# Performance work log

Hardware: AMD Instinct MI355X
Metric: run time of the kernel (lower is better)

The kernel has to match this reference:

```python
import jax, jax.numpy as jnp
import numpy as np

# ---- static config (from init_kwargs) ----
SAMPLE_RATE = 2048.0
MAX_SHIFT = int(0.025 * SAMPLE_RATE)          # 51 samples
NUM_BINS = 16
FFTLENGTH = 1.0                               # chisq_kernel_length (s)
DF = 1.0 / FFTLENGTH
NUM_FREQS = int(FFTLENGTH * SAMPLE_RATE // 2 + 1)   # 1025 == rfft bins of 2048 samples
HIGHPASS = 32.0
CHISQ_PENALTY = 1.0
_freqs = np.arange(NUM_FREQS) / FFTLENGTH
MASK = _freqs >= HIGHPASS                     # static numpy bool mask

BATCH, CHANNELS, DIM = 256, 2, 2048


def setup_inputs() -> dict:
    key = jax.random.key(0)
    k1, k2 = jax.random.split(key)
    x_hat = jax.random.normal(k1, (BATCH, CHANNELS, DIM), dtype=jnp.float32)
    x = jax.random.normal(k2, (BATCH, CHANNELS, DIM), dtype=jnp.float32)
    return {"x_hat": x_hat, "x": x}


def _center(x):
    xmin = x.min(-1, keepdims=True)
    xmax = x.max(-1, keepdims=True)
    return 2 * (x - xmin) / (xmax - xmin) - 1


def _shifted_pearson(x, y, max_shift):
    # x, y: [B, C, T]; returns corr: [W, B, C] with W = 2*max_shift + 1
    b, c, t = x.shape
    num_windows = 2 * max_shift + 1
    xp = jnp.pad(x, ((0, 0), (0, 0), (max_shift, max_shift)))
    # window w, position i -> xp[..., i + w]  (same layout as torch unfold)
    idx = jnp.arange(num_windows)[:, None] + jnp.arange(t)[None, :]   # [W, T]
    xw = xp[:, :, idx]                                                # [B, C, W, T]
    xw = jnp.transpose(xw, (2, 0, 1, 3))                              # [W, B, C, T]
    xw = xw - xw.mean(-1, keepdims=True)
    yc = y - y.mean(-1, keepdims=True)
    corr = (xw * yc).sum(-1)
    norm = (xw ** 2).sum(-1) * (yc ** 2).sum(-1)
    return corr / jnp.sqrt(norm)


def _snr_integral(a, b):
    # |4 * a * conj(b) * df| cumulatively summed over frequency
    integrand = a * jnp.conj(b)
    return jnp.abs(4 * integrand * DF).cumsum(-1)


def _chisq(htilde, stilde):
    htilde = htilde[:, :, MASK]
    stilde = stilde[:, :, MASK]
    # partition frequencies by the template's own optimal-SNR integral
    si = _snr_integral(htilde, htilde)                    # [B, C, F]
    total = si[:, :, -1:]
    bins = (jnp.arange(NUM_BINS + 1, dtype=si.dtype) / NUM_BINS) * total  # [B, C, NB+1]
    search = jax.vmap(jax.vmap(lambda a, v: jnp.searchsorted(a, v, side="right")))
    edges = search(si, bins)
    edges = jnp.clip(edges, 0, si.shape[-1] - 1)
    qtilde = htilde / jnp.sqrt(total).astype(htilde.dtype)
    # SNR per bin of the normalized template against the strain
    si2 = _snr_integral(qtilde, stilde)                   # [B, C, F]
    total2 = si2[:, :, -1:]
    right = jnp.take_along_axis(si2, edges[:, :, 1:], axis=-1)
    left = jnp.take_along_axis(si2, edges[:, :, :-1], axis=-1)
    snr_per_bin = right - left                            # [B, C, NB]
    summand = (snr_per_bin - total2 / NUM_BINS) ** 2
    chisq = NUM_BINS * summand.sum(-1) / (NUM_BINS - 1)
    return total2[:, :, 0], chisq


def reference(x_hat, x):
    x_hat = _center(x_hat)
    corr = _shifted_pearson(x_hat, x, MAX_SHIFT)          # [W, B, C]
    corr = corr.max(0)                                    # [B, C]
    loss = (1 - corr) / (1 + corr)
    htilde = jnp.fft.rfft(x_hat, axis=-1) / SAMPLE_RATE   # [B, C, 1025] complex
    stilde = jnp.fft.rfft(x, axis=-1) / SAMPLE_RATE
    _, chisq = _chisq(htilde, stilde)
    chisq = chisq * CHISQ_PENALTY
    loss = loss * (1 + chisq ** 3) ** (1.0 / 6.0)
    return loss
```

## Files before the change

### kernel.cpp

```cpp
#include <hip/hip_runtime.h>
#include <math.h>

#define ROWS 512
#define DIM 2048
#define MS 51
#define NWIN 103
#define KMIN 32
#define NMASK 993
#define PHYS(i) ((i) + ((i) >> 5))

__global__ __launch_bounds__(512) void fused_mfl_kernel(
    const float* __restrict__ xhat, const float* __restrict__ x,
    float* __restrict__ out)
{
    const int r = blockIdx.x;
    const int t = threadIdx.x;
    const int lane = t & 63;
    const int wave = t >> 6;
    const float* xh = xhat + (size_t)r * DIM;
    const float* xr = x + (size_t)r * DIM;

    __shared__ float smem[16384];
    float* red6  = smem;
    float* yh    = smem;
    float* yc    = smem + 2224;
    float* headS = smem + 4352;
    float* headQ = smem + 4404;
    float* tailS = smem + 4456;
    float* tailQ = smem + 4508;
    float* V     = smem + 9216;
    float* corrv = smem + 16220;
    float2* A  = (float2*)smem;
    float2* Bb = (float2*)(smem + 4096);
    float2* TW = (float2*)(smem + 8192);
    float* siA  = smem;
    float* siBr = smem + 1024;

    __shared__ float sc[8];
    __shared__ int   edges[17];
    __shared__ float summ[16];
    __shared__ float wsA[8], wsB[8];

    float4 a4 = ((const float4*)xh)[t];
    float4 b4 = ((const float4*)xr)[t];
    float av[4] = {a4.x, a4.y, a4.z, a4.w};
    float bv[4] = {b4.x, b4.y, b4.z, b4.w};

    {
        float swv, cwv;
        sincosf((float)t * (-3.14159265358979323846f / 1024.0f), &swv, &cwv);
        TW[t] = make_float2(cwv, swv);
    }

    {
        float mn4 = fminf(fminf(av[0], av[1]), fminf(av[2], av[3]));
        float mx4 = fmaxf(fmaxf(av[0], av[1]), fmaxf(av[2], av[3]));
        float sa = (av[0] + av[1]) + (av[2] + av[3]);
        float qa = (av[0]*av[0] + av[1]*av[1]) + (av[2]*av[2] + av[3]*av[3]);
        float sx = (bv[0] + bv[1]) + (bv[2] + bv[3]);
        float qx = (bv[0]*bv[0] + bv[1]*bv[1]) + (bv[2]*bv[2] + bv[3]*bv[3]);
        red6[t]        = mn4;
        red6[512 + t]  = mx4;
        red6[1024 + t] = sa;
        red6[1536 + t] = qa;
        red6[2048 + t] = sx;
        red6[2560 + t] = qx;
    }
    __syncthreads();
    if (wave == 0) {
        float4 u, v;
        u = ((const float4*)(red6       ))[2*lane]; v = ((const float4*)(red6       ))[2*lane+1];
        float pmn = fminf(fminf(fminf(u.x,u.y),fminf(u.z,u.w)),
                          fminf(fminf(v.x,v.y),fminf(v.z,v.w)));
        u = ((const float4*)(red6 +  512))[2*lane]; v = ((const float4*)(red6 +  512))[2*lane+1];
        float pmx = fmaxf(fmaxf(fmaxf(u.x,u.y),fmaxf(u.z,u.w)),
                          fmaxf(fmaxf(v.x,v.y),fmaxf(v.z,v.w)));
        u = ((const float4*)(red6 + 1024))[2*lane]; v = ((const float4*)(red6 + 1024))[2*lane+1];
        float psa = ((u.x+u.y)+(u.z+u.w)) + ((v.x+v.y)+(v.z+v.w));
        u = ((const float4*)(red6 + 1536))[2*lane]; v = ((const float4*)(red6 + 1536))[2*lane+1];
        float pqa = ((u.x+u.y)+(u.z+u.w)) + ((v.x+v.y)+(v.z+v.w));
        u = ((const float4*)(red6 + 2048))[2*lane]; v = ((const float4*)(red6 + 2048))[2*lane+1];
        float psx = ((u.x+u.y)+(u.z+u.w)) + ((v.x+v.y)+(v.z+v.w));
        u = ((const float4*)(red6 + 2560))[2*lane]; v = ((const float4*)(red6 + 2560))[2*lane+1];
        float pqx = ((u.x+u.y)+(u.z+u.w)) + ((v.x+v.y)+(v.z+v.w));
#pragma unroll
        for (int d = 32; d; d >>= 1) {
            pmn = fminf(pmn, __shfl_down(pmn, d));
            pmx = fmaxf(pmx, __shfl_down(pmx, d));
            psa += __shfl_down(psa, d);
            pqa += __shfl_down(pqa, d);
            psx += __shfl_down(psx, d);
            pqx += __shfl_down(pqx, d);
        }
        if (lane == 0) {
            float mn = pmn, mx = pmx;
            float scl = 2.0f / (mx - mn);
            float mean = psx * (1.0f / DIM);
            float Sm = psa - (float)DIM * mn;
            float S1 = scl * Sm - (float)DIM;
            float S2 = scl * scl * (pqa - 2.f * mn * psa + (float)DIM * mn * mn)
                     - 2.f * scl * Sm + (float)DIM;
            float Syy = pqx - (float)DIM * mean * mean;
            sc[0] = mn; sc[1] = scl; sc[2] = mean;
            sc[3] = S1; sc[4] = S2; sc[5] = Syy;
        }
    }
    __syncthreads();
    const float mnv = sc[0], scl = sc[1], mean = sc[2];
    const float S1 = sc[3], S2 = sc[4], Syy = sc[5];

    float yhv[4];
#pragma unroll
    for (int j = 0; j < 4; ++j) {
        float y = (av[j] - mnv) * scl - 1.0f;
        float z = bv[j] - mean;
        yhv[j] = y;
        int i = 4 * t + j;
        yh[PHYS(i + MS)] = y;
        yc[PHYS(i)] = z;
    }
    if (t < MS) { yh[PHYS(t)] = 0.f; yh[PHYS(t + MS + DIM)] = 0.f; }
    __syncthreads();

    if (wave < 2) {
        float v = 0.f;
        if (lane >= 1 && lane <= MS)
            v = (wave == 0) ? yh[PHYS(MS + lane - 1)] : yh[PHYS(MS + DIM - lane)];
        float s = v, q = v * v;
#pragma unroll
        for (int d = 1; d < 64; d <<= 1) {
            float ys = __shfl_up(s, d);
            float yq = __shfl_up(q, d);
            if (lane >= d) { s += ys; q += yq; }
        }
        if (lane <= MS) {
            if (wave == 0) { headS[lane] = s; headQ[lane] = q; }
            else           { tailS[lane] = s; tailQ[lane] = q; }
        }
    }

    float ycr[32];
#pragma unroll
    for (int j = 0; j < 32; ++j) ycr[j] = yc[PHYS(32 * lane + j)];

    const int c0 = 13 * wave;
    const int base0 = 32 * lane + c0;
    float wreg[32];
#pragma unroll
    for (int j = 0; j < 32; ++j) wreg[j] = yh[PHYS(base0 + j)];

    float pacc[13];
#pragma unroll
    for (int i = 0; i < 13; ++i) {
        float acc = 0.f;
#pragma unroll
        for (int j = 0; j < 32; ++j) acc += wreg[(i + j) & 31] * ycr[j];
        pacc[i] = acc;
        if (i < 12) wreg[i & 31] = yh[PHYS(base0 + 32 + i)];
    }
#pragma unroll
    for (int i = 0; i < 13; ++i) {
        int c = c0 + i;
        if (c < NWIN) V[68 * c + lane] = pacc[i];
    }
    __syncthreads();

    if (t < 4 * NWIN) {
        int c = t >> 2, k = t & 3;
        const float4* vp = (const float4*)(V + 68 * c + 16 * k);
        float4 u0 = vp[0], u1 = vp[1], u2 = vp[2], u3 = vp[3];
        float acc = ((u0.x+u0.y)+(u0.z+u0.w)) + ((u1.x+u1.y)+(u1.z+u1.w))
                  + ((u2.x+u2.y)+(u2.z+u2.w)) + ((u3.x+u3.y)+(u3.z+u3.w));
        acc += __shfl_down(acc, 1);
        acc += __shfl_down(acc, 2);
        if (k == 0) {
            int off = c - MS;
            float sw, qw;
            if (off >= 0) { sw = S1 - headS[off]; qw = S2 - headQ[off]; }
            else          { sw = S1 - tailS[-off]; qw = S2 - tailQ[-off]; }
            float varw = qw - sw * sw * (1.0f / DIM);
            corrv[c] = acc / sqrtf(varw * Syy);
        }
    }
#pragma unroll
    for (int j = 0; j < 4; ++j) A[4 * t + j] = make_float2(yhv[j], bv[j]);
    __syncthreads();

    if (wave == 0) {
        float m = (lane < NWIN) ? corrv[lane] : -2.0f;
        if (lane + 64 < NWIN) m = fmaxf(m, corrv[lane + 64]);
#pragma unroll
        for (int d = 32; d; d >>= 1) m = fmaxf(m, __shfl_down(m, d));
        if (lane == 0) sc[6] = (1.0f - m) / (1.0f + m);
    }

    float2 *S = A, *D = Bb;
#pragma unroll
    for (int stage = 0; stage < 5; ++stage) {
        const int s = 1 << (2 * stage);
        const int q = t;
        const int u = q & ~(s - 1);
        float2 x0 = S[q];
        float2 x1 = S[q + 512];
        float2 x2 = S[q + 1024];
        float2 x3 = S[q + 1536];
        float t0r = x0.x + x2.x, t0i = x0.y + x2.y;
        float t1r = x0.x - x2.x, t1i = x0.y - x2.y;
        float t2r = x1.x + x3.x, t2i = x1.y + x3.y;
        float d3r = x1.x - x3.x, d3i = x1.y - x3.y;
        float t3r = d3i, t3i = -d3r;
        float2 w1 = TW[u];
        float w2r = w1.x * w1.x - w1.y * w1.y, w2i = 2.f * w1.x * w1.y;
        float w3r = w2r * w1.x - w2i * w1.y,  w3i = w2r * w1.y + w2i * w1.x;
        float y0r = t0r + t2r, y0i = t0i + t2i;
        float a1r = t1r + t3r, a1i = t1i + t3i;
        float y1r = a1r * w1.x - a1i * w1.y, y1i = a1r * w1.y + a1i * w1.x;
        float a2r = t0r - t2r, a2i = t0i - t2i;
        float y2r = a2r * w2r - a2i * w2i, y2i = a2r * w2i + a2i * w2r;
        float a3r = t1r - t3r, a3i = t1i - t3i;
        float y3r = a3r * w3r - a3i * w3i, y3i = a3r * w3i + a3i * w3r;
        int base = q + 3 * u;
        D[base]         = make_float2(y0r, y0i);
        D[base + s]     = make_float2(y1r, y1i);
        D[base + 2 * s] = make_float2(y2r, y2i);
        D[base + 3 * s] = make_float2(y3r, y3i);
        __syncthreads();
        float2* tmp = S; S = D; D = tmp;
    }

    const float MSC = 0.5f * (1.0f / 2048.0f);
    float h[2], sg[2];
#pragma unroll
    for (int j = 0; j < 2; ++j) {
        int m = 2 * t + j;
        if (m < NMASK) {
            int f = m + KMIN;
            float zfr, zfi;
            if (f < 1024) {
                float2 p = S[f], q2 = S[f + 1024];
                zfr = p.x + q2.x; zfi = p.y + q2.y;
            } else {
                float2 p = S[0], q2 = S[1024];
                zfr = p.x - q2.x; zfi = p.y - q2.y;
            }
            int g = 2048 - f;
            float2 p2 = S[g - 1024], q3 = S[g];
            float zgr = p2.x - q3.x, zgi = p2.y - q3.y;
            float hre = zfr + zgr, him = zfi - zgi;
            float sre = zfi + zgi, sim = zgr - zfr;
            h[j]  = sqrtf(hre * hre + him * him) * MSC;
            sg[j] = sqrtf(sre * sre + sim * sim) * MSC;
        } else { h[j] = 0.f; sg[j] = 0.f; }
    }

    float e0 = 4.f * h[0] * h[0];
    float e1 = e0 + 4.f * h[1] * h[1];
    float g0 = 4.f * h[0] * sg[0];
    float g1 = g0 + 4.f * h[1] * sg[1];
    float totE = e1, totG = g1;
    float incE = totE, incG = totG;
#pragma unroll
    for (int d = 1; d < 64; d <<= 1) {
        float yE = __shfl_up(incE, d);
        float yG = __shfl_up(incG, d);
        if (lane >= d) { incE += yE; incG += yG; }
    }
    if (lane == 63) { wsA[wave] = incE; wsB[wave] = incG; }
    __syncthreads();
    float offE = 0.f, offG = 0.f;
    for (int w = 0; w < wave; ++w) { offE += wsA[w]; offG += wsB[w]; }
    float preE = offE + incE - totE;
    float preG = offG + incG - totG;
    siA[2 * t]      = preE + e0;
    siA[2 * t + 1]  = preE + e1;
    siBr[2 * t]     = preG + g0;
    siBr[2 * t + 1] = preG + g1;
    __syncthreads();
    const float total  = siA[NMASK - 1];
    const float qf     = 1.0f / sqrtf(total);
    const float total2 = siBr[NMASK - 1] * qf;

    if (t < 17) {
        float bin = ((float)t * (1.0f / 16.0f)) * total;
        int lo = 0, hi = NMASK;
        while (lo < hi) {
            int mid = (lo + hi) >> 1;
            if (siA[mid] <= bin) lo = mid + 1; else hi = mid;
        }
        edges[t] = (lo < NMASK - 1) ? lo : (NMASK - 1);
    }
    __syncthreads();

    if (t < 16) {
        float snr = (siBr[edges[t + 1]] - siBr[edges[t]]) * qf;
        float d = snr - total2 * (1.0f / 16.0f);
        summ[t] = d * d;
    }
    __syncthreads();
    if (t == 0) {
        float ssum = 0.f;
        for (int i = 0; i < 16; ++i) ssum += summ[i];
        float chisq = 16.0f * ssum / 15.0f;
        float c3 = chisq * chisq * chisq;
        out[r] = sc[6] * powf(1.0f + c3, 1.0f / 6.0f);
    }
}

extern "C" void kernel_launch(void* const* d_in, const int* in_sizes, int n_in,
                              void* d_out, int out_size, void* d_ws, size_t ws_size,
                              hipStream_t stream) {
    const float* xhat = (const float*)d_in[0];
    const float* x    = (const float*)d_in[1];
    float* out = (float*)d_out;
    (void)in_sizes; (void)n_in; (void)out_size; (void)d_ws; (void)ws_size;

    fused_mfl_kernel<<<ROWS, 512, 0, stream>>>(xhat, x, out);
}
```

Baseline: 69.95 us.

## Compute shifted cross-correlation via inverse FFT of spectrum product instead of direct dot products

```diff
diff --git a/kernel.cpp b/kernel.cpp
--- a/kernel.cpp
+++ b/kernel.cpp
@@ -7,7 +7,7 @@
 #define NWIN 103
 #define KMIN 32
 #define NMASK 993
-#define PHYS(i) ((i) + ((i) >> 5))
+#define INVS (1.0f/8192.0f)
 
 __global__ __launch_bounds__(512) void fused_mfl_kernel(
     const float* __restrict__ xhat, const float* __restrict__ x,
@@ -20,21 +20,22 @@
     const float* xh = xhat + (size_t)r * DIM;
     const float* xr = x + (size_t)r * DIM;
 
-    __shared__ float smem[16384];
-    float* red6  = smem;
-    float* yh    = smem;
-    float* yc    = smem + 2224;
-    float* headS = smem + 4352;
-    float* headQ = smem + 4404;
-    float* tailS = smem + 4456;
-    float* tailQ = smem + 4508;
-    float* V     = smem + 9216;
-    float* corrv = smem + 16220;
+    __shared__ float smem[11780];
     float2* A  = (float2*)smem;
     float2* Bb = (float2*)(smem + 4096);
     float2* TW = (float2*)(smem + 8192);
-    float* siA  = smem;
-    float* siBr = smem + 1024;
+    float* red6  = smem;
+    float* siA   = smem + 9216;
+    float* siBr  = smem + 10240;
+    float* headS = smem + 11264;
+    float* headQ = smem + 11316;
+    float* tailS = smem + 11368;
+    float* tailQ = smem + 11420;
+    float* yhH   = smem + 11472;
+    float* yhT   = smem + 11523;
+    float* ycH   = smem + 11574;
+    float* ycT   = smem + 11625;
+    float* corrv = smem + 11676;
 
     __shared__ float sc[8];
     __shared__ int   edges[17];
@@ -51,6 +52,35 @@
         sincosf((float)t * (-3.14159265358979323846f / 1024.0f), &swv, &cwv);
         TW[t] = make_float2(cwv, swv);
     }
+
+    auto fft_stage = [&](const float2* Sp, float2* Dp, const int s) {
+        const int q = t;
+        const int u = q & ~(s - 1);
+        float2 x0 = Sp[q];
+        float2 x1 = Sp[q + 512];
+        float2 x2 = Sp[q + 1024];
+        float2 x3 = Sp[q + 1536];
+        float t0r = x0.x + x2.x, t0i = x0.y + x2.y;
+        float t1r = x0.x - x2.x, t1i = x0.y - x2.y;
+        float t2r = x1.x + x3.x, t2i = x1.y + x3.y;
+        float d3r = x1.x - x3.x, d3i = x1.y - x3.y;
+        float t3r = d3i, t3i = -d3r;
+        float2 w1 = TW[u];
+        float w2r = w1.x * w1.x - w1.y * w1.y, w2i = 2.f * w1.x * w1.y;
+        float w3r = w2r * w1.x - w2i * w1.y,  w3i = w2r * w1.y + w2i * w1.x;
+        float y0r = t0r + t2r, y0i = t0i + t2i;
+        float a1r = t1r + t3r, a1i = t1i + t3i;
+        float y1r = a1r * w1.x - a1i * w1.y, y1i = a1r * w1.y + a1i * w1.x;
+        float a2r = t0r - t2r, a2i = t0i - t2i;
+        float y2r = a2r * w2r - a2i * w2i, y2i = a2r * w2i + a2i * w2r;
+        float a3r = t1r - t3r, a3i = t1i - t3i;
+        float y3r = a3r * w3r - a3i * w3i, y3i = a3r * w3i + a3i * w3r;
+        int base = q + 3 * u;
+        Dp[base]         = make_float2(y0r, y0i);
+        Dp[base + s]     = make_float2(y1r, y1i);
+        Dp[base + 2 * s] = make_float2(y2r, y2i);
+        Dp[base + 3 * s] = make_float2(y3r, y3i);
+    };
 
     {
         float mn4 = fminf(fminf(av[0], av[1]), fminf(av[2], av[3]));
@@ -97,35 +127,33 @@
             float scl = 2.0f / (mx - mn);
             float mean = psx * (1.0f / DIM);
             float Sm = psa - (float)DIM * mn;
-            float S1 = scl * Sm - (float)DIM;
-            float S2 = scl * scl * (pqa - 2.f * mn * psa + (float)DIM * mn * mn)
-                     - 2.f * scl * Sm + (float)DIM;
-            float Syy = pqx - (float)DIM * mean * mean;
+            float S1v = scl * Sm - (float)DIM;
+            float S2v = scl * scl * (pqa - 2.f * mn * psa + (float)DIM * mn * mn)
+                      - 2.f * scl * Sm + (float)DIM;
+            float Syyv = pqx - (float)DIM * mean * mean;
             sc[0] = mn; sc[1] = scl; sc[2] = mean;
-            sc[3] = S1; sc[4] = S2; sc[5] = Syy;
+            sc[3] = S1v; sc[4] = S2v; sc[5] = Syyv;
         }
     }
     __syncthreads();
     const float mnv = sc[0], scl = sc[1], mean = sc[2];
     const float S1 = sc[3], S2 = sc[4], Syy = sc[5];
 
-    float yhv[4];
 #pragma unroll
     for (int j = 0; j < 4; ++j) {
+        int i = 4 * t + j;
         float y = (av[j] - mnv) * scl - 1.0f;
         float z = bv[j] - mean;
-        yhv[j] = y;
-        int i = 4 * t + j;
-        yh[PHYS(i + MS)] = y;
-        yc[PHYS(i)] = z;
-    }
-    if (t < MS) { yh[PHYS(t)] = 0.f; yh[PHYS(t + MS + DIM)] = 0.f; }
+        A[i] = make_float2(y, bv[j]);
+        if (i < MS)        { yhH[i] = y;        ycH[i] = z; }
+        if (i >= DIM - MS) { yhT[i - (DIM - MS)] = y; ycT[i - (DIM - MS)] = z; }
+    }
     __syncthreads();
 
     if (wave < 2) {
         float v = 0.f;
         if (lane >= 1 && lane <= MS)
-            v = (wave == 0) ? yh[PHYS(MS + lane - 1)] : yh[PHYS(MS + DIM - lane)];
+            v = (wave == 0) ? yhH[lane - 1] : yhT[MS - lane];
         float s = v, q = v * v;
 #pragma unroll
         for (int d = 1; d < 64; d <<= 1) {
@@ -139,94 +167,11 @@
         }
     }
 
-    float ycr[32];
-#pragma unroll
-    for (int j = 0; j < 32; ++j) ycr[j] = yc[PHYS(32 * lane + j)];
-
-    const int c0 = 13 * wave;
-    const int base0 = 32 * lane + c0;
-    float wreg[32];
-#pragma unroll
-    for (int j = 0; j < 32; ++j) wreg[j] = yh[PHYS(base0 + j)];
-
-    float pacc[13];
-#pragma unroll
-    for (int i = 0; i < 13; ++i) {
-        float acc = 0.f;
-#pragma unroll
-        for (int j = 0; j < 32; ++j) acc += wreg[(i + j) & 31] * ycr[j];
-        pacc[i] = acc;
-        if (i < 12) wreg[i & 31] = yh[PHYS(base0 + 32 + i)];
-    }
-#pragma unroll
-    for (int i = 0; i < 13; ++i) {
-        int c = c0 + i;
-        if (c < NWIN) V[68 * c + lane] = pacc[i];
-    }
-    __syncthreads();
-
-    if (t < 4 * NWIN) {
-        int c = t >> 2, k = t & 3;
-        const float4* vp = (const float4*)(V + 68 * c + 16 * k);
-        float4 u0 = vp[0], u1 = vp[1], u2 = vp[2], u3 = vp[3];
-        float acc = ((u0.x+u0.y)+(u0.z+u0.w)) + ((u1.x+u1.y)+(u1.z+u1.w))
-                  + ((u2.x+u2.y)+(u2.z+u2.w)) + ((u3.x+u3.y)+(u3.z+u3.w));
-        acc += __shfl_down(acc, 1);
-        acc += __shfl_down(acc, 2);
-        if (k == 0) {
-            int off = c - MS;
-            float sw, qw;
-            if (off >= 0) { sw = S1 - headS[off]; qw = S2 - headQ[off]; }
-            else          { sw = S1 - tailS[-off]; qw = S2 - tailQ[-off]; }
-            float varw = qw - sw * sw * (1.0f / DIM);
-            corrv[c] = acc / sqrtf(varw * Syy);
-        }
-    }
-#pragma unroll
-    for (int j = 0; j < 4; ++j) A[4 * t + j] = make_float2(yhv[j], bv[j]);
-    __syncthreads();
-
-    if (wave == 0) {
-        float m = (lane < NWIN) ? corrv[lane] : -2.0f;
-        if (lane + 64 < NWIN) m = fmaxf(m, corrv[lane + 64]);
-#pragma unroll
-        for (int d = 32; d; d >>= 1) m = fmaxf(m, __shfl_down(m, d));
-        if (lane == 0) sc[6] = (1.0f - m) / (1.0f + m);
-    }
-
-    float2 *S = A, *D = Bb;
-#pragma unroll
-    for (int stage = 0; stage < 5; ++stage) {
-        const int s = 1 << (2 * stage);
-        const int q = t;
-        const int u = q & ~(s - 1);
-        float2 x0 = S[q];
-        float2 x1 = S[q + 512];
-        float2 x2 = S[q + 1024];
-        float2 x3 = S[q + 1536];
-        float t0r = x0.x + x2.x, t0i = x0.y + x2.y;
-        float t1r = x0.x - x2.x, t1i = x0.y - x2.y;
-        float t2r = x1.x + x3.x, t2i = x1.y + x3.y;
-        float d3r = x1.x - x3.x, d3i = x1.y - x3.y;
-        float t3r = d3i, t3i = -d3r;
-        float2 w1 = TW[u];
-        float w2r = w1.x * w1.x - w1.y * w1.y, w2i = 2.f * w1.x * w1.y;
-        float w3r = w2r * w1.x - w2i * w1.y,  w3i = w2r * w1.y + w2i * w1.x;
-        float y0r = t0r + t2r, y0i = t0i + t2i;
-        float a1r = t1r + t3r, a1i = t1i + t3i;
-        float y1r = a1r * w1.x - a1i * w1.y, y1i = a1r * w1.y + a1i * w1.x;
-        float a2r = t0r - t2r, a2i = t0i - t2i;
-        float y2r = a2r * w2r - a2i * w2i, y2i = a2r * w2i + a2i * w2r;
-        float a3r = t1r - t3r, a3i = t1i - t3i;
-        float y3r = a3r * w3r - a3i * w3i, y3i = a3r * w3i + a3i * w3r;
-        int base = q + 3 * u;
-        D[base]         = make_float2(y0r, y0i);
-        D[base + s]     = make_float2(y1r, y1i);
-        D[base + 2 * s] = make_float2(y2r, y2i);
-        D[base + 3 * s] = make_float2(y3r, y3i);
-        __syncthreads();
-        float2* tmp = S; S = D; D = tmp;
-    }
+    fft_stage(A, Bb, 1);    __syncthreads();
+    fft_stage(Bb, A, 4);    __syncthreads();
+    fft_stage(A, Bb, 16);   __syncthreads();
+    fft_stage(Bb, A, 64);   __syncthreads();
+    fft_stage(A, Bb, 256);  __syncthreads();
 
     const float MSC = 0.5f * (1.0f / 2048.0f);
     float h[2], sg[2];
@@ -237,21 +182,42 @@
             int f = m + KMIN;
             float zfr, zfi;
             if (f < 1024) {
-                float2 p = S[f], q2 = S[f + 1024];
+                float2 p = Bb[f], q2 = Bb[f + 1024];
                 zfr = p.x + q2.x; zfi = p.y + q2.y;
             } else {
-                float2 p = S[0], q2 = S[1024];
+                float2 p = Bb[0], q2 = Bb[1024];
                 zfr = p.x - q2.x; zfi = p.y - q2.y;
             }
             int g = 2048 - f;
-            float2 p2 = S[g - 1024], q3 = S[g];
+            float2 p2 = Bb[g - 1024], q3 = Bb[g];
             float zgr = p2.x - q3.x, zgi = p2.y - q3.y;
             float hre = zfr + zgr, him = zfi - zgi;
             float sre = zfi + zgi, sim = zgr - zfr;
             h[j]  = sqrtf(hre * hre + him * him) * MSC;
             sg[j] = sqrtf(sre * sre + sim * sim) * MSC;
+            float pr = hre * sre + him * sim;
+            float pi = him * sre - hre * sim;
+            A[f] = make_float2(pr, -pi);
+            if (f < 1024) A[2048 - f] = make_float2(pr, pi);
         } else { h[j] = 0.f; sg[j] = 0.f; }
     }
+    if (t < 32) {
+        if (t == 0) A[0] = make_float2(0.f, 0.f);
+        else {
+            int f = t;
+            float2 p = Bb[f], q2 = Bb[f + 1024];
+            float zfr = p.x + q2.x, zfi = p.y + q2.y;
+            float2 p2 = Bb[1024 - f], q3 = Bb[2048 - f];
+            float zgr = p2.x - q3.x, zgi = p2.y - q3.y;
+            float hre = zfr + zgr, him = zfi - zgi;
+            float sre = zfi + zgi, sim = zgr - zfr;
+            float pr = hre * sre + him * sim;
+            float pi = him * sre - hre * sim;
+            A[f] = make_float2(pr, -pi);
+            A[2048 - f] = make_float2(pr, pi);
+        }
+    }
+    __syncthreads();
 
     float e0 = 4.f * h[0] * h[0];
     float e1 = e0 + 4.f * h[1] * h[1];
@@ -266,20 +232,25 @@
         if (lane >= d) { incE += yE; incG += yG; }
     }
     if (lane == 63) { wsA[wave] = incE; wsB[wave] = incG; }
-    __syncthreads();
-    float offE = 0.f, offG = 0.f;
-    for (int w = 0; w < wave; ++w) { offE += wsA[w]; offG += wsB[w]; }
-    float preE = offE + incE - totE;
-    float preG = offG + incG - totG;
-    siA[2 * t]      = preE + e0;
-    siA[2 * t + 1]  = preE + e1;
-    siBr[2 * t]     = preG + g0;
-    siBr[2 * t + 1] = preG + g1;
-    __syncthreads();
+    fft_stage(A, Bb, 1);
+    __syncthreads();
+
+    {
+        float offE = 0.f, offG = 0.f;
+        for (int w = 0; w < wave; ++w) { offE += wsA[w]; offG += wsB[w]; }
+        float preE = offE + incE - totE;
+        float preG = offG + incG - totG;
+        siA[2 * t]      = preE + e0;
+        siA[2 * t + 1]  = preE + e1;
+        siBr[2 * t]     = preG + g0;
+        siBr[2 * t + 1] = preG + g1;
+    }
+    fft_stage(Bb, A, 4);
+    __syncthreads();
+
     const float total  = siA[NMASK - 1];
     const float qf     = 1.0f / sqrtf(total);
     const float total2 = siBr[NMASK - 1] * qf;
-
     if (t < 17) {
         float bin = ((float)t * (1.0f / 16.0f)) * total;
         int lo = 0, hi = NMASK;
@@ -289,6 +260,7 @@
         }
         edges[t] = (lo < NMASK - 1) ? lo : (NMASK - 1);
     }
+    fft_stage(A, Bb, 16);
     __syncthreads();
 
     if (t < 16) {
@@ -296,13 +268,50 @@
         float d = snr - total2 * (1.0f / 16.0f);
         summ[t] = d * d;
     }
-    __syncthreads();
-    if (t == 0) {
-        float ssum = 0.f;
-        for (int i = 0; i < 16; ++i) ssum += summ[i];
-        float chisq = 16.0f * ssum / 15.0f;
-        float c3 = chisq * chisq * chisq;
-        out[r] = sc[6] * powf(1.0f + c3, 1.0f / 6.0f);
+    fft_stage(Bb, A, 64);
+    __syncthreads();
+
+    fft_stage(A, Bb, 256);
+    __syncthreads();
+
+    if (t < 4 * NWIN) {
+        int c = t >> 2, k = t & 3;
+        int off = c - MS;
+        float acc = 0.f;
+        if (off > 0) {
+            for (int j = k; j < off; j += 4) acc += yhH[j] * ycT[MS - off + j];
+        } else if (off < 0) {
+            for (int j = k; j < -off; j += 4) acc += yhT[MS + off + j] * ycH[j];
+        }
+        acc += __shfl_down(acc, 1);
+        acc += __shfl_down(acc, 2);
+        if (k == 0) {
+            int sidx = (off >= 0) ? off : (2048 + off);
+            float cc = (sidx < 1024) ? (Bb[sidx].x + Bb[sidx + 1024].x)
+                                     : (Bb[sidx - 1024].x - Bb[sidx].x);
+            float num = cc * INVS - acc;
+            float sw, qw;
+            if (off >= 0) { sw = S1 - headS[off];  qw = S2 - headQ[off]; }
+            else          { sw = S1 - tailS[-off]; qw = S2 - tailQ[-off]; }
+            float varw = qw - sw * sw * (1.0f / DIM);
+            corrv[c] = num / sqrtf(varw * Syy);
+        }
+    }
+    __syncthreads();
+
+    if (wave == 0) {
+        float m = (lane < NWIN) ? corrv[lane] : -2.0f;
+        if (lane + 64 < NWIN) m = fmaxf(m, corrv[lane + 64]);
+#pragma unroll
+        for (int d = 32; d; d >>= 1) m = fmaxf(m, __shfl_down(m, d));
+        if (lane == 0) {
+            float loss0 = (1.0f - m) / (1.0f + m);
+            float ssum = 0.f;
+            for (int i = 0; i < 16; ++i) ssum += summ[i];
+            float chisq = 16.0f * ssum / 15.0f;
+            float c3 = chisq * chisq * chisq;
+            out[r] = loss0 * powf(1.0f + c3, 1.0f / 6.0f);
+        }
     }
 }
 
```

Result: faster. 68.43 us (-2.2%).
